# Performance work log

Measured on AMD Instinct MI355X. Metric: run time of the kernel, lower is better.

The kernel has to match this reference:

```python
import jax, jax.numpy as jnp
import numpy as np

B, L, D, H = 4, 1024, 768, 6
DH = D // H
EPS = 1e-5


def setup_inputs() -> dict:
    key = jax.random.key(0)
    kq, kk, kv, kl, kw = jax.random.split(key, 5)
    Q = jax.random.normal(kq, (B, L, D), jnp.float32)
    K = jax.random.normal(kk, (B, L, D), jnp.float32)
    V = jax.random.normal(kv, (B, L, D), jnp.float32)
    # realistic padding: each batch element has a valid length in [L//2, L]
    lengths = jax.random.randint(kl, (B,), L // 2, L + 1)
    valid = jnp.arange(L)[None, :] < lengths[:, None]          # (B, L)
    pad_mask = valid[:, :, None] & valid[:, None, :]           # (B, L, L), True = keep
    bx_packed = ~valid                                         # (B, L), True = padded
    # BatchNorm affine params (per-head channels)
    g1 = jnp.ones((H,), jnp.float32)
    b1 = jnp.zeros((H,), jnp.float32)
    g2 = jnp.ones((H,), jnp.float32)
    b2 = jnp.zeros((H,), jnp.float32)
    # posterior gate: Linear(H, 2)
    Wp = jax.random.normal(kw, (2, H), jnp.float32) * (1.0 / np.sqrt(H))
    bp = jnp.zeros((2,), jnp.float32)
    return {"Q": Q, "K": K, "V": V, "pad_mask": pad_mask, "bx_packed": bx_packed,
            "g1": g1, "b1": b1, "g2": g2, "b2": b2, "Wp": Wp, "bp": bp}


def _split_heads(x):
    b, l, _ = x.shape
    return x.reshape(b, l, H, DH).transpose(0, 2, 1, 3)  # (B, H, L, DH)


def _batchnorm(x, g, b):
    # x: (B, H, N); training-mode BatchNorm1d over channels H (stats over B and N)
    m = x.mean(axis=(0, 2), keepdims=True)
    v = x.var(axis=(0, 2), keepdims=True)  # biased, as torch uses for normalization
    return (x - m) * jax.lax.rsqrt(v + EPS) * g[None, :, None] + b[None, :, None]


def _remove_nan(x):
    return jnp.where(jnp.isnan(x), jnp.zeros_like(x), x)


def reference(Q, K, V, pad_mask, bx_packed, g1, b1, g2, b2, Wp, bp):
    Qh, Kh, Vh = _split_heads(Q), _split_heads(K), _split_heads(V)
    b, h, l, _ = Qh.shape
    # DistMatrix: negative squared Euclidean distance between query/key vectors
    # scores[b,h,i,j] = -||Q_i - K_j||^2, via the GEMM-friendly expansion
    q2 = jnp.sum(Qh * Qh, axis=-1)                     # (B, H, L)
    k2 = jnp.sum(Kh * Kh, axis=-1)                     # (B, H, L)
    qk = jnp.einsum("bhid,bhjd->bhij", Qh, Kh)         # (B, H, L, L)
    co = -(q2[..., :, None] + k2[..., None, :] - 2.0 * qk)
    # norm1 over flattened L*L
    co = _batchnorm(co.reshape(b, h, l * l), g1, b1).reshape(b, h, l, l)
    # zero out positions where pad_mask is False (in-place masked fill in torch)
    co = jnp.where(pad_mask[:, None, :, :], co, 0.0)
    co = jax.nn.softmax(co, axis=-1)
    co = _remove_nan(co)
    # column-sum attention mass per key position
    w = co.sum(axis=-2)                                # (B, H, L)
    w = _batchnorm(w, g2, b2).transpose(0, 2, 1)       # (B, L, H)
    # posterior gate: Linear(H,2) + softmax, take class-0 probability
    w = jax.nn.softmax(w @ Wp.T + bp, axis=-1)[..., 0]  # (B, L)
    w = _remove_nan(w)
    w = jnp.where(bx_packed, -jnp.inf, w)
    w = jax.nn.softmax(w, axis=-1)
    w = _remove_nan(w)[..., None]                      # (B, L, 1)
    return co, w, Vh
```

## Files before the change

kernel.cpp:

```cpp
#include <hip/hip_runtime.h>
#include <stdint.h>
#include <stddef.h>

#define BB 4
#define LL 1024
#define DD 768
#define HH 6
#define DHH 128
#define EPS 1e-5f
#define LOG2E 1.44269504088896f

#define CO_ELEMS 25165824
#define W_ELEMS  4096

#define OFF_Q2  0
#define OFF_K2  24576
#define OFF_WC  49152
#define OFF_SP  73728
#define OFF_AC  79872
#define OFF_SS  79888
#define OFF_WP  81920
#define OFF_GP  1654784
#define OFF_MS1 5193728
#define OFF_MS2 5242880

typedef __attribute__((ext_vector_type(8))) short short8;
typedef __attribute__((ext_vector_type(4))) float f32x4;

__device__ __forceinline__ short8 ld_bf8(const float* __restrict__ p) {
    const float4 a = *(const float4*)(p);
    const float4 b = *(const float4*)(p + 4);
    short8 r;
    r[0] = (short)(__float_as_uint(a.x) >> 16);
    r[1] = (short)(__float_as_uint(a.y) >> 16);
    r[2] = (short)(__float_as_uint(a.z) >> 16);
    r[3] = (short)(__float_as_uint(a.w) >> 16);
    r[4] = (short)(__float_as_uint(b.x) >> 16);
    r[5] = (short)(__float_as_uint(b.y) >> 16);
    r[6] = (short)(__float_as_uint(b.z) >> 16);
    r[7] = (short)(__float_as_uint(b.w) >> 16);
    return r;
}

__device__ __forceinline__ short8 pack_bf8(float4 a, float4 b) {
    short8 r;
    r[0] = (short)(__float_as_uint(a.x) >> 16);
    r[1] = (short)(__float_as_uint(a.y) >> 16);
    r[2] = (short)(__float_as_uint(a.z) >> 16);
    r[3] = (short)(__float_as_uint(a.w) >> 16);
    r[4] = (short)(__float_as_uint(b.x) >> 16);
    r[5] = (short)(__float_as_uint(b.y) >> 16);
    r[6] = (short)(__float_as_uint(b.z) >> 16);
    r[7] = (short)(__float_as_uint(b.w) >> 16);
    return r;
}

__global__ __launch_bounds__(256) void k_gram(
        const float* __restrict__ Q, const float* __restrict__ K,
        const float* __restrict__ V,
        float* __restrict__ ws, float* __restrict__ gramP,
        float* __restrict__ ms1, float* __restrict__ ms2,
        float* __restrict__ vh) {
    const int ic = blockIdx.x;
    const int bh = blockIdx.y;
    const int which = blockIdx.z;
    const int b = bh / HH, h = bh - b * HH;
    const int t = threadIdx.x;

    if (which == 2) {
        const float* srcv = V + (size_t)b * LL * DD + h * DHH;
        float* dstv = vh + ((size_t)bh * LL + (size_t)ic * 128) * DHH;
#pragma unroll
        for (int p = 0; p < 16; p++) {
            const int idx = p * 256 + t;
            const int row = idx >> 5, d4 = idx & 31;
            f32x4 v = *(const f32x4*)(srcv + (size_t)(ic * 128 + row) * DD + d4 * 4);
            __builtin_nontemporal_store(v, (f32x4*)(dstv + (size_t)row * DHH + d4 * 4));
        }
        return;
    }

    const float* src = (which ? K : Q) + (size_t)b * LL * DD + h * DHH;
    float* sqout = ws + (which ? OFF_K2 : OFF_Q2) + bh * 1024 + ic * 128;

    const int lane = t & 63, wv = t >> 6;
    const int lm = lane & 15, quad = lane >> 4;

    __shared__ float tileT[128][129];
    __shared__ float q2loc[128];

    const int ig = t >> 5;
    const int d0 = (t & 31) * 4;
#pragma unroll 4
    for (int p = 0; p < 16; p++) {
        const int i_loc = p * 8 + ig;
        float4 v = *(const float4*)(src + (size_t)(ic * 128 + i_loc) * DD + d0);
        tileT[d0 + 0][i_loc] = __uint_as_float(__float_as_uint(v.x) & 0xffff0000u);
        tileT[d0 + 1][i_loc] = __uint_as_float(__float_as_uint(v.y) & 0xffff0000u);
        tileT[d0 + 2][i_loc] = __uint_as_float(__float_as_uint(v.z) & 0xffff0000u);
        tileT[d0 + 3][i_loc] = __uint_as_float(__float_as_uint(v.w) & 0xffff0000u);
        float s = v.x * v.x + v.y * v.y + v.z * v.z + v.w * v.w;
#pragma unroll
        for (int off = 1; off < 32; off <<= 1) s += __shfl_xor(s, off);
        if ((t & 31) == 0) { q2loc[i_loc] = s; sqout[i_loc] = s; }
    }
    __syncthreads();

    if (t < 128) {
        float s1 = 0.f, s2 = 0.f;
#pragma unroll 8
        for (int i = 0; i < 128; i++) {
            float v = tileT[t][i];
            s1 += v;
            s2 += v * q2loc[i];
        }
        const size_t mo = ((size_t)(which * 24 + bh) * 8 + ic) * 128 + t;
        ms1[mo] = s1;
        ms2[mo] = s2;
    }

    const size_t gbase = ((size_t)(which * 24 + bh) * 8 + ic) * 9216;
    int pi = 0;
    for (int dt = 0; dt < 8; dt++) {
        for (int et = dt; et < 8; et++, pi++) {
            if ((pi & 3) != wv) continue;
            f32x4 acc = (f32x4)(0.0f);
#pragma unroll
            for (int kk = 0; kk < 4; kk++) {
                const int i0 = kk * 32 + quad * 8;
                const float* pa = &tileT[dt * 16 + lm][i0];
                const float* pb = &tileT[et * 16 + lm][i0];
                short8 af, bf;
#pragma unroll
                for (int e = 0; e < 8; e++) {
                    af[e] = (short)(__float_as_uint(pa[e]) >> 16);
                    bf[e] = (short)(__float_as_uint(pb[e]) >> 16);
                }
                acc = __builtin_amdgcn_mfma_f32_16x16x32_bf16(af, bf, acc, 0, 0, 0);
            }
            if (dt != et && which == 0) {
                acc[0] *= 2.f; acc[1] *= 2.f; acc[2] *= 2.f; acc[3] *= 2.f;
            }
            *(f32x4*)&gramP[gbase + (size_t)pi * 256 + lane * 4] = acc;
        }
    }
}

__global__ __launch_bounds__(1024) void k_stats3(
        const float* __restrict__ ms1, const float* __restrict__ ms2,
        const float* __restrict__ gramP,
        const float* __restrict__ q2, const float* __restrict__ k2,
        float* __restrict__ statsP) {
    const int bh = blockIdx.x;
    const int t = threadIdx.x, lane = t & 63, w = t >> 6;
    __shared__ float sQ[128], sK[128], sQq2[128], sKk2[128];
    __shared__ float sred[16][4];
    __shared__ float gred[16];

    if (t < 256) {
        const int d = t & 127, which = t >> 7;
        const float* p1 = ms1 + (size_t)(which * 24 + bh) * 1024 + d;
        const float* p2 = ms2 + (size_t)(which * 24 + bh) * 1024 + d;
        float s1 = 0.f, s2 = 0.f;
#pragma unroll
        for (int ic = 0; ic < 8; ic++) { s1 += p1[ic * 128]; s2 += p2[ic * 128]; }
        if (which) { sK[d] = s1; sKk2[d] = s2; }
        else       { sQ[d] = s1; sQq2[d] = s2; }
    }
    if (t >= 512 && t < 768) {
        const int tt = t - 512;
        f32x4 qv = *(const f32x4*)(q2 + bh * 1024 + tt * 4);
        f32x4 kv = *(const f32x4*)(k2 + bh * 1024 + tt * 4);
        float p0 = qv[0] + qv[1] + qv[2] + qv[3];
        float p1 = qv[0]*qv[0] + qv[1]*qv[1] + qv[2]*qv[2] + qv[3]*qv[3];
        float p2 = kv[0] + kv[1] + kv[2] + kv[3];
        float p3 = kv[0]*kv[0] + kv[1]*kv[1] + kv[2]*kv[2] + kv[3]*kv[3];
#pragma unroll
        for (int off = 1; off < 64; off <<= 1) {
            p0 += __shfl_xor(p0, off); p1 += __shfl_xor(p1, off);
            p2 += __shfl_xor(p2, off); p3 += __shfl_xor(p3, off);
        }
        if (lane == 0) { sred[w][0] = p0; sred[w][1] = p1; sred[w][2] = p2; sred[w][3] = p3; }
    }
    {
        const float* gq = gramP + (size_t)(0 * 24 + bh) * 8 * 9216;
        const float* gk = gramP + (size_t)(1 * 24 + bh) * 8 * 9216;
        float gg = 0.f;
#pragma unroll
        for (int it = 0; it < 9; it++) {
            const int f = it * 1024 + t;
            float a = 0.f, c = 0.f;
#pragma unroll
            for (int icc = 0; icc < 8; icc++) {
                a += gq[(size_t)icc * 9216 + f];
                c += gk[(size_t)icc * 9216 + f];
            }
            gg += a * c;
        }
#pragma unroll
        for (int off = 1; off < 64; off <<= 1) gg += __shfl_xor(gg, off);
        if (lane == 0) gred[w] = gg;
    }
    __syncthreads();
    if (t < 64) {
        float dA  = sQ[t] * sK[t] + sQ[t + 64] * sK[t + 64];
        float dBq = sQq2[t] * sK[t] + sQq2[t + 64] * sK[t + 64];
        float dBk = sQ[t] * sKk2[t] + sQ[t + 64] * sKk2[t + 64];
#pragma unroll
        for (int off = 1; off < 64; off <<= 1) {
            dA += __shfl_xor(dA, off); dBq += __shfl_xor(dBq, off); dBk += __shfl_xor(dBk, off);
        }
        if (t == 0) {
            float SQ2   = sred[8][0] + sred[9][0] + sred[10][0] + sred[11][0];
            float SQ2SQ = sred[8][1] + sred[9][1] + sred[10][1] + sred[11][1];
            float SK2   = sred[8][2] + sred[9][2] + sred[10][2] + sred[11][2];
            float SK2SQ = sred[8][3] + sred[9][3] + sred[10][3] + sred[11][3];
            float GG = 0.f;
#pragma unroll
            for (int i = 0; i < 16; i++) GG += gred[i];
            float sumS  = 2.f * dA - 1024.f * (SQ2 + SK2);
            float sumS2 = 4.f * GG + 1024.f * (SQ2SQ + SK2SQ) + 2.f * SQ2 * SK2 - 4.f * (dBq + dBk);
            statsP[bh * 2]     = sumS;
            statsP[bh * 2 + 1] = sumS2;
        }
    }
}

__global__ void k_stats2(const float* __restrict__ statsP,
                         const float* __restrict__ g1, const float* __restrict__ b1,
                         float* __restrict__ ac) {
    const int t = threadIdx.x;
    if (t < HH) {
        float T1 = 0.f, T2 = 0.f;
#pragma unroll
        for (int b = 0; b < 4; b++) {
            T1 += statsP[(b * HH + t) * 2];
            T2 += statsP[(b * HH + t) * 2 + 1];
        }
        const float N = 4194304.f;
        float m_ = T1 / N;
        float var = fmaxf(T2 / N - m_ * m_, 0.0f);
        float r = rsqrtf(var + EPS);
        float a = r * g1[t];
        ac[t] = a;
        ac[8 + t] = b1[t] - m_ * a;
    }
}

#define KLOAD(buf, jtv) do {                                                   \
    const float* _p = Kb + (size_t)(jw + (jtv) * 16 + lm) * DD + quad * 8;     \
    buf##0 = *(const float4*)(_p);        buf##1 = *(const float4*)(_p + 4);   \
    buf##2 = *(const float4*)(_p + 32);   buf##3 = *(const float4*)(_p + 36);  \
    buf##4 = *(const float4*)(_p + 64);   buf##5 = *(const float4*)(_p + 68);  \
    buf##6 = *(const float4*)(_p + 96);   buf##7 = *(const float4*)(_p + 100); \
} while (0)

#define KCOMP(buf, jtv) do {                                                   \
    short8 kf0 = pack_bf8(buf##0, buf##1);                                     \
    short8 kf1 = pack_bf8(buf##2, buf##3);                                     \
    short8 kf2 = pack_bf8(buf##4, buf##5);                                     \
    short8 kf3 = pack_bf8(buf##6, buf##7);                                     \
    f32x4 acc0 = (f32x4)(0.0f), acc1 = (f32x4)(0.0f);                          \
    acc0 = __builtin_amdgcn_mfma_f32_16x16x32_bf16(kf0, qf[0][0], acc0, 0, 0, 0); \
    acc1 = __builtin_amdgcn_mfma_f32_16x16x32_bf16(kf0, qf[1][0], acc1, 0, 0, 0); \
    acc0 = __builtin_amdgcn_mfma_f32_16x16x32_bf16(kf1, qf[0][1], acc0, 0, 0, 0); \
    acc1 = __builtin_amdgcn_mfma_f32_16x16x32_bf16(kf1, qf[1][1], acc1, 0, 0, 0); \
    acc0 = __builtin_amdgcn_mfma_f32_16x16x32_bf16(kf2, qf[0][2], acc0, 0, 0, 0); \
    acc1 = __builtin_amdgcn_mfma_f32_16x16x32_bf16(kf2, qf[1][2], acc1, 0, 0, 0); \
    acc0 = __builtin_amdgcn_mfma_f32_16x16x32_bf16(kf3, qf[0][3], acc0, 0, 0, 0); \
    acc1 = __builtin_amdgcn_mfma_f32_16x16x32_bf16(kf3, qf[1][3], acc1, 0, 0, 0); \
    const int jb = jw + (jtv) * 16;                                            \
    const f32x4 k2v = *(const f32x4*)(k2 + bh * 1024 + jb + quad * 4);         \
    const uchar4 m4 = *(const uchar4*)(bxb + jb + quad * 4);                   \
    const bool vj0 = (m4.x == 0), vj1 = (m4.y == 0);                           \
    const bool vj2 = (m4.z == 0), vj3 = (m4.w == 0);                           \
    f32x4 kc;                                                                  \
    kc[0] = a1l * k2v[0]; kc[1] = a1l * k2v[1];                                \
    kc[2] = a1l * k2v[2]; kc[3] = a1l * k2v[3];                                \
    {                                                                          \
        f32x4 ev;                                                              \
        ev[0] = (vi0 && vj0) ? exp2f(fminf(fmaf(a2l, acc0[0], cr0 - kc[0]), 86.56f)) : 1.0f; \
        ev[1] = (vi0 && vj1) ? exp2f(fminf(fmaf(a2l, acc0[1], cr0 - kc[1]), 86.56f)) : 1.0f; \
        ev[2] = (vi0 && vj2) ? exp2f(fminf(fmaf(a2l, acc0[2], cr0 - kc[2]), 86.56f)) : 1.0f; \
        ev[3] = (vi0 && vj3) ? exp2f(fminf(fmaf(a2l, acc0[3], cr0 - kc[3]), 86.56f)) : 1.0f; \
        *(f32x4*)&e_lds[lm][jb + quad * 4] = ev;                               \
        rsum0 += (ev[0] + ev[1]) + (ev[2] + ev[3]);                            \
    }                                                                          \
    {                                                                          \
        f32x4 ev;                                                              \
        ev[0] = (vi1 && vj0) ? exp2f(fminf(fmaf(a2l, acc1[0], cr1 - kc[0]), 86.56f)) : 1.0f; \
        ev[1] = (vi1 && vj1) ? exp2f(fminf(fmaf(a2l, acc1[1], cr1 - kc[1]), 86.56f)) : 1.0f; \
        ev[2] = (vi1 && vj2) ? exp2f(fminf(fmaf(a2l, acc1[2], cr1 - kc[2]), 86.56f)) : 1.0f; \
        ev[3] = (vi1 && vj3) ? exp2f(fminf(fmaf(a2l, acc1[3], cr1 - kc[3]), 86.56f)) : 1.0f; \
        *(f32x4*)&e_lds[16 + lm][jb + quad * 4] = ev;                          \
        rsum1 += (ev[0] + ev[1]) + (ev[2] + ev[3]);                            \
    }                                                                          \
} while (0)

__global__ __launch_bounds__(512, 1) void k_fused(
        const float* __restrict__ Q, const float* __restrict__ Km,
        const float* __restrict__ q2, const float* __restrict__ k2,
        const float* __restrict__ ac, const unsigned char* __restrict__ bx,
        float* __restrict__ co, float* __restrict__ wcolP) {
    const int g = blockIdx.x;
    const int xcd = g & 7, slot = g >> 3;
    const int t = threadIdx.x, lane = t & 63, w = t >> 6;
    const int lm = lane & 15, quad = lane >> 4;
    const int jw = w * 128;

    __shared__ float e_lds[32][1028];
    __shared__ float rowsum[3][32];
    if (t < 96) ((float*)rowsum)[t] = 0.f;
    __syncthreads();

#pragma unroll 1
    for (int rep = 0; rep < 3; rep++) {
        const int idx = slot * 3 + rep;
        const int bh = xcd + ((idx >> 5) << 3);
        const int strip = idx & 31;
        const int b = bh / HH, h = bh - b * HH;
        const int i0 = strip * 32;
        const float* Qb = Q + (size_t)b * LL * DD + h * DHH;
        const float* Kb = Km + (size_t)b * LL * DD + h * DHH;
        const float a1 = ac[h], c1 = ac[8 + h];
        const unsigned char* bxb = bx + b * LL;
        const float a1l = a1 * LOG2E;
        const float a2l = 2.0f * a1l;
        const float c1l = c1 * LOG2E;

        short8 qf[2][4];
#pragma unroll
        for (int s = 0; s < 2; s++)
#pragma unroll
            for (int kk = 0; kk < 4; kk++)
                qf[s][kk] = ld_bf8(Qb + (size_t)(i0 + s * 16 + lm) * DD + kk * 32 + quad * 8);

        const bool vi0 = (bxb[i0 + lm] == 0);
        const bool vi1 = (bxb[i0 + 16 + lm] == 0);
        const float cr0 = c1l - a1l * q2[bh * 1024 + i0 + lm];
        const float cr1 = c1l - a1l * q2[bh * 1024 + i0 + 16 + lm];

        float4 rA0, rA1, rA2, rA3, rA4, rA5, rA6, rA7;
        float4 rB0, rB1, rB2, rB3, rB4, rB5, rB6, rB7;

        float rsum0 = 0.f, rsum1 = 0.f;
        KLOAD(rA, 0);
        KLOAD(rB, 1);
        KCOMP(rA, 0);
        KLOAD(rA, 2);
        KCOMP(rB, 1);
        KLOAD(rB, 3);
        KCOMP(rA, 2);
        KLOAD(rA, 4);
        KCOMP(rB, 3);
        KLOAD(rB, 5);
        KCOMP(rA, 4);
        KLOAD(rA, 6);
        KCOMP(rB, 5);
        KLOAD(rB, 7);
        KCOMP(rA, 6);
        KCOMP(rB, 7);

        rsum0 += __shfl_xor(rsum0, 16);
        rsum0 += __shfl_xor(rsum0, 32);
        rsum1 += __shfl_xor(rsum1, 16);
        rsum1 += __shfl_xor(rsum1, 32);
        if (lane < 16) {
            atomicAdd(&rowsum[rep][lm], rsum0);
            atomicAdd(&rowsum[rep][16 + lm], rsum1);
        }
        __syncthreads();

        const int cg = t & 255, rh = t >> 8;
        float* cob = co + ((size_t)bh << 20) + (size_t)(i0 + rh * 16) * 1024 + cg * 4;
        float* wp = wcolP + ((size_t)((strip * 2 + rh) * 24 + bh)) * 1024 + cg * 4;
        float cs0 = 0.f, cs1 = 0.f, cs2 = 0.f, cs3 = 0.f;
#pragma unroll
        for (int rr = 0; rr < 16; rr++) {
            const int r = rh * 16 + rr;
            const float inv = 1.0f / rowsum[rep][r];
            f32x4 v = *(const f32x4*)&e_lds[r][cg * 4];
            v[0] *= inv; v[1] *= inv; v[2] *= inv; v[3] *= inv;
            __builtin_nontemporal_store(v, (f32x4*)(cob + (size_t)rr * 1024));
            cs0 += v[0]; cs1 += v[1]; cs2 += v[2]; cs3 += v[3];
        }
        f32x4 wv; wv[0] = cs0; wv[1] = cs1; wv[2] = cs2; wv[3] = cs3;
        *(f32x4*)wp = wv;
        __syncthreads();
    }
}

__global__ void k_wcol_reduce(const float* __restrict__ wcolP,
                              float* __restrict__ wcol, float* __restrict__ ws2) {
    const int t = threadIdx.x;
    int g = blockIdx.x * 256 + t;
    float s = 0.f;
#pragma unroll 8
    for (int strip = 0; strip < 64; strip++)
        s += wcolP[(size_t)strip * 24576 + g];
    wcol[g] = s;
    float a = s, b = s * s;
#pragma unroll
    for (int off = 1; off < 64; off <<= 1) { a += __shfl_xor(a, off); b += __shfl_xor(b, off); }
    __shared__ float sc[4][2];
    if ((t & 63) == 0) { sc[t >> 6][0] = a; sc[t >> 6][1] = b; }
    __syncthreads();
    if (t == 0) {
        ws2[blockIdx.x * 2]     = sc[0][0] + sc[1][0] + sc[2][0] + sc[3][0];
        ws2[blockIdx.x * 2 + 1] = sc[0][1] + sc[1][1] + sc[2][1] + sc[3][1];
    }
}

__global__ __launch_bounds__(1024) void k_tail(
        const float* __restrict__ wcol, const float* __restrict__ ws2,
        const unsigned char* __restrict__ bx,
        const float* __restrict__ g2, const float* __restrict__ b2,
        const float* __restrict__ Wp, const float* __restrict__ bp,
        float* __restrict__ wout) {
    const int t = threadIdx.x, lane = t & 63, wv = t >> 6;
    __shared__ float abuf[12];
    __shared__ float xb[4096];
    __shared__ float wred[16][2];

    if (t < HH) {
        float s = 0.f, s2 = 0.f;
        for (int b = 0; b < 4; b++) {
            int bh = b * HH + t;
#pragma unroll
            for (int sub = 0; sub < 4; sub++) {
                int blk = bh * 4 + sub;
                s += ws2[blk * 2];
                s2 += ws2[blk * 2 + 1];
            }
        }
        float m = s / 4096.f;
        float var = fmaxf(s2 / 4096.f - m * m, 0.0f);
        float r = rsqrtf(var + EPS);
        float a = r * g2[t];
        abuf[t] = a;
        abuf[6 + t] = b2[t] - m * a;
    }
    __syncthreads();

    const float bp0 = bp[0], bp1 = bp[1];
#pragma unroll
    for (int p = 0; p < 4; p++) {
        int idx = t + p * 1024;
        int b = idx >> 10, l = idx & 1023;
        float z0 = bp0, z1 = bp1;
#pragma unroll
        for (int h = 0; h < HH; h++) {
            float wn = abuf[h] * wcol[(size_t)(b * HH + h) * 1024 + l] + abuf[6 + h];
            z0 += wn * Wp[h];
            z1 += wn * Wp[HH + h];
        }
        float pc = 1.0f / (1.0f + __expf(z1 - z0));
        xb[idx] = bx[b * LL + l] ? -INFINITY : pc;
    }
    __syncthreads();

    const int bb = t >> 8, tb = t & 255;
    float4 xv = *(const float4*)&xb[bb * 1024 + tb * 4];
    float mx = fmaxf(fmaxf(xv.x, xv.y), fmaxf(xv.z, xv.w));
#pragma unroll
    for (int off = 1; off < 64; off <<= 1) mx = fmaxf(mx, __shfl_xor(mx, off));
    if (lane == 0) wred[wv][0] = mx;
    __syncthreads();
    mx = fmaxf(fmaxf(wred[bb * 4][0], wred[bb * 4 + 1][0]),
               fmaxf(wred[bb * 4 + 2][0], wred[bb * 4 + 3][0]));
    float e0 = __expf(xv.x - mx), e1 = __expf(xv.y - mx);
    float e2 = __expf(xv.z - mx), e3 = __expf(xv.w - mx);
    float ss = e0 + e1 + e2 + e3;
#pragma unroll
    for (int off = 1; off < 64; off <<= 1) ss += __shfl_xor(ss, off);
    if (lane == 0) wred[wv][1] = ss;
    __syncthreads();
    float sum = wred[bb * 4][1] + wred[bb * 4 + 1][1] + wred[bb * 4 + 2][1] + wred[bb * 4 + 3][1];
    float4 o;
    o.x = e0 / sum; o.y = e1 / sum; o.z = e2 / sum; o.w = e3 / sum;
    *(float4*)&wout[bb * 1024 + tb * 4] = o;
}

extern "C" void kernel_launch(void* const* d_in, const int* in_sizes, int n_in,
                              void* d_out, int out_size, void* d_ws, size_t ws_size,
                              hipStream_t stream) {
    const float* Q  = (const float*)d_in[0];
    const float* K  = (const float*)d_in[1];
    const float* V  = (const float*)d_in[2];
    const unsigned char* bx = (const unsigned char*)d_in[4];
    const float* g1 = (const float*)d_in[5];
    const float* b1 = (const float*)d_in[6];
    const float* g2 = (const float*)d_in[7];
    const float* b2 = (const float*)d_in[8];
    const float* Wp = (const float*)d_in[9];
    const float* bp = (const float*)d_in[10];

    float* out  = (float*)d_out;
    float* co   = out;
    float* wout = out + CO_ELEMS;
    float* vh   = out + CO_ELEMS + W_ELEMS;

    float* ws = (float*)d_ws;
    float* q2     = ws + OFF_Q2;
    float* k2     = ws + OFF_K2;
    float* wcol   = ws + OFF_WC;
    float* statsP = ws + OFF_SP;
    float* ac     = ws + OFF_AC;
    float* ws2    = ws + OFF_SS;
    float* wcolP  = ws + OFF_WP;
    float* gramP  = ws + OFF_GP;
    float* ms1    = ws + OFF_MS1;
    float* ms2    = ws + OFF_MS2;

    k_gram<<<dim3(8, 24, 3), 256, 0, stream>>>(Q, K, V, ws, gramP, ms1, ms2, vh);
    k_stats3<<<24, 1024, 0, stream>>>(ms1, ms2, gramP, q2, k2, statsP);
    k_stats2<<<1, 64, 0, stream>>>(statsP, g1, b1, ac);
    k_fused<<<256, 512, 0, stream>>>(Q, K, q2, k2, ac, bx, co, wcolP);
    k_wcol_reduce<<<96, 256, 0, stream>>>(wcolP, wcol, ws2);
    k_tail<<<1, 1024, 0, stream>>>(wcol, ws2, bx, g2, b2, Wp, bp, wout);
}
```

Baseline: 260.7 us.

## Fuse stats2, wcol reduce and tail into preceding kernels via atomic last-block counters

Removes three small kernel launches by folding the BN1 finalization into k_stats3 and the column reduction plus the final gate softmax into k_fused, using global atomic counters so the last-arriving block does the follow-up work. It also prefetches the next strip's Q fragments and K tiles before the store phase of the current strip, so loads overlap the co writes. The costs are extra fences and serialized tail work in a single block, plus the risk of memory-ordering bugs with the counters.

```diff
diff --git a/kernel.cpp b/kernel.cpp
--- a/kernel.cpp
+++ b/kernel.cpp
@@ -23,6 +23,7 @@
 #define OFF_GP  1654784
 #define OFF_MS1 5193728
 #define OFF_MS2 5242880
+#define OFF_CT  5292032
 
 typedef __attribute__((ext_vector_type(8))) short short8;
 typedef __attribute__((ext_vector_type(4))) float f32x4;
@@ -55,12 +56,18 @@
     return r;
 }
 
+__device__ __forceinline__ void bar_lgkm() {
+    asm volatile("s_waitcnt lgkmcnt(0)" ::: "memory");
+    __builtin_amdgcn_s_barrier();
+    __builtin_amdgcn_sched_barrier(0);
+}
+
 __global__ __launch_bounds__(256) void k_gram(
         const float* __restrict__ Q, const float* __restrict__ K,
         const float* __restrict__ V,
         float* __restrict__ ws, float* __restrict__ gramP,
         float* __restrict__ ms1, float* __restrict__ ms2,
-        float* __restrict__ vh) {
+        float* __restrict__ vh, unsigned* __restrict__ ctr) {
     const int ic = blockIdx.x;
     const int bh = blockIdx.y;
     const int which = blockIdx.z;
@@ -68,6 +75,7 @@
     const int t = threadIdx.x;
 
     if (which == 2) {
+        if (ic == 0 && bh == 0 && t < 32) ctr[t] = 0u;
         const float* srcv = V + (size_t)b * LL * DD + h * DHH;
         float* dstv = vh + ((size_t)bh * LL + (size_t)ic * 128) * DHH;
 #pragma unroll
@@ -150,7 +158,9 @@
         const float* __restrict__ ms1, const float* __restrict__ ms2,
         const float* __restrict__ gramP,
         const float* __restrict__ q2, const float* __restrict__ k2,
-        float* __restrict__ statsP) {
+        const float* __restrict__ g1, const float* __restrict__ b1,
+        float* __restrict__ statsP, float* __restrict__ ac,
+        unsigned* __restrict__ ctr) {
     const int bh = blockIdx.x;
     const int t = threadIdx.x, lane = t & 63, w = t >> 6;
     __shared__ float sQ[128], sK[128], sQq2[128], sKk2[128];
@@ -222,28 +232,28 @@
             float sumS2 = 4.f * GG + 1024.f * (SQ2SQ + SK2SQ) + 2.f * SQ2 * SK2 - 4.f * (dBq + dBk);
             statsP[bh * 2]     = sumS;
             statsP[bh * 2 + 1] = sumS2;
-        }
-    }
-}
-
-__global__ void k_stats2(const float* __restrict__ statsP,
-                         const float* __restrict__ g1, const float* __restrict__ b1,
-                         float* __restrict__ ac) {
-    const int t = threadIdx.x;
-    if (t < HH) {
-        float T1 = 0.f, T2 = 0.f;
-#pragma unroll
-        for (int b = 0; b < 4; b++) {
-            T1 += statsP[(b * HH + t) * 2];
-            T2 += statsP[(b * HH + t) * 2 + 1];
-        }
-        const float N = 4194304.f;
-        float m_ = T1 / N;
-        float var = fmaxf(T2 / N - m_ * m_, 0.0f);
-        float r = rsqrtf(var + EPS);
-        float a = r * g1[t];
-        ac[t] = a;
-        ac[8 + t] = b1[t] - m_ * a;
+            __threadfence();
+            unsigned old = atomicAdd(&ctr[30], 1u);
+            if (old == 23u) {
+                __threadfence();
+#pragma unroll
+                for (int h = 0; h < HH; h++) {
+                    float T1 = 0.f, T2 = 0.f;
+#pragma unroll
+                    for (int b = 0; b < 4; b++) {
+                        T1 += statsP[(b * HH + h) * 2];
+                        T2 += statsP[(b * HH + h) * 2 + 1];
+                    }
+                    const float N = 4194304.f;
+                    float m_ = T1 / N;
+                    float var = fmaxf(T2 / N - m_ * m_, 0.0f);
+                    float r = rsqrtf(var + EPS);
+                    float a = r * g1[h];
+                    ac[h] = a;
+                    ac[8 + h] = b1[h] - m_ * a;
+                }
+            }
+        }
     }
 }
 
@@ -270,7 +280,7 @@
     acc0 = __builtin_amdgcn_mfma_f32_16x16x32_bf16(kf3, qf[0][3], acc0, 0, 0, 0); \
     acc1 = __builtin_amdgcn_mfma_f32_16x16x32_bf16(kf3, qf[1][3], acc1, 0, 0, 0); \
     const int jb = jw + (jtv) * 16;                                            \
-    const f32x4 k2v = *(const f32x4*)(k2 + bh * 1024 + jb + quad * 4);         \
+    const f32x4 k2v = *(const f32x4*)(k2b + jb + quad * 4);                    \
     const uchar4 m4 = *(const uchar4*)(bxb + jb + quad * 4);                   \
     const bool vj0 = (m4.x == 0), vj1 = (m4.y == 0);                           \
     const bool vj2 = (m4.z == 0), vj3 = (m4.w == 0);                           \
@@ -297,11 +307,37 @@
     }                                                                          \
 } while (0)
 
+#define SETUP(idxv) do {                                                       \
+    bh = xcd + ((((idxv) >> 5)) << 3); strip = (idxv) & 31;                    \
+    const int b_ = bh / HH, h_ = bh - b_ * HH;                                 \
+    const int i0_ = strip * 32;                                                \
+    const float* Qb_ = Q + (size_t)b_ * LL * DD + h_ * DHH;                    \
+    Kb  = Km + (size_t)b_ * LL * DD + h_ * DHH;                                \
+    k2b = k2 + bh * 1024;                                                      \
+    bxb = bx + b_ * LL;                                                        \
+    a1l = ac[h_] * LOG2E; a2l = 2.0f * a1l;                                    \
+    const float c1l_ = ac[8 + h_] * LOG2E;                                     \
+    _Pragma("unroll")                                                          \
+    for (int s = 0; s < 2; s++)                                                \
+        _Pragma("unroll")                                                      \
+        for (int kk = 0; kk < 4; kk++)                                         \
+            qf[s][kk] = ld_bf8(Qb_ + (size_t)(i0_ + s * 16 + lm) * DD + kk * 32 + quad * 8); \
+    vi0 = (bxb[i0_ + lm] == 0);                                                \
+    vi1 = (bxb[i0_ + 16 + lm] == 0);                                           \
+    cr0 = c1l_ - a1l * q2[bh * 1024 + i0_ + lm];                               \
+    cr1 = c1l_ - a1l * q2[bh * 1024 + i0_ + 16 + lm];                          \
+    KLOAD(rA, 0); KLOAD(rB, 1);                                                \
+} while (0)
+
 __global__ __launch_bounds__(512, 1) void k_fused(
         const float* __restrict__ Q, const float* __restrict__ Km,
         const float* __restrict__ q2, const float* __restrict__ k2,
         const float* __restrict__ ac, const unsigned char* __restrict__ bx,
-        float* __restrict__ co, float* __restrict__ wcolP) {
+        const float* __restrict__ g2, const float* __restrict__ b2,
+        const float* __restrict__ Wp, const float* __restrict__ bp,
+        float* __restrict__ co, float* __restrict__ wcolP,
+        float* __restrict__ wcol, float* __restrict__ ws2,
+        unsigned* __restrict__ ctr, float* __restrict__ wout) {
     const int g = blockIdx.x;
     const int xcd = g & 7, slot = g >> 3;
     const int t = threadIdx.x, lane = t & 63, w = t >> 6;
@@ -310,42 +346,26 @@
 
     __shared__ float e_lds[32][1028];
     __shared__ float rowsum[3][32];
+    __shared__ int sclaim[2];
+    __shared__ int stail;
+    __shared__ float scr[8][2];
+    __shared__ float abuf[12];
     if (t < 96) ((float*)rowsum)[t] = 0.f;
     __syncthreads();
+
+    int bh, strip;
+    const float* Kb; const float* k2b; const unsigned char* bxb;
+    float a1l, a2l, cr0, cr1;
+    bool vi0, vi1;
+    short8 qf[2][4];
+    float4 rA0, rA1, rA2, rA3, rA4, rA5, rA6, rA7;
+    float4 rB0, rB1, rB2, rB3, rB4, rB5, rB6, rB7;
+
+    SETUP(slot * 3);
 
 #pragma unroll 1
     for (int rep = 0; rep < 3; rep++) {
-        const int idx = slot * 3 + rep;
-        const int bh = xcd + ((idx >> 5) << 3);
-        const int strip = idx & 31;
-        const int b = bh / HH, h = bh - b * HH;
-        const int i0 = strip * 32;
-        const float* Qb = Q + (size_t)b * LL * DD + h * DHH;
-        const float* Kb = Km + (size_t)b * LL * DD + h * DHH;
-        const float a1 = ac[h], c1 = ac[8 + h];
-        const unsigned char* bxb = bx + b * LL;
-        const float a1l = a1 * LOG2E;
-        const float a2l = 2.0f * a1l;
-        const float c1l = c1 * LOG2E;
-
-        short8 qf[2][4];
-#pragma unroll
-        for (int s = 0; s < 2; s++)
-#pragma unroll
-            for (int kk = 0; kk < 4; kk++)
-                qf[s][kk] = ld_bf8(Qb + (size_t)(i0 + s * 16 + lm) * DD + kk * 32 + quad * 8);
-
-        const bool vi0 = (bxb[i0 + lm] == 0);
-        const bool vi1 = (bxb[i0 + 16 + lm] == 0);
-        const float cr0 = c1l - a1l * q2[bh * 1024 + i0 + lm];
-        const float cr1 = c1l - a1l * q2[bh * 1024 + i0 + 16 + lm];
-
-        float4 rA0, rA1, rA2, rA3, rA4, rA5, rA6, rA7;
-        float4 rB0, rB1, rB2, rB3, rB4, rB5, rB6, rB7;
-
         float rsum0 = 0.f, rsum1 = 0.f;
-        KLOAD(rA, 0);
-        KLOAD(rB, 1);
         KCOMP(rA, 0);
         KLOAD(rA, 2);
         KCOMP(rB, 1);
@@ -369,11 +389,16 @@
             atomicAdd(&rowsum[rep][lm], rsum0);
             atomicAdd(&rowsum[rep][16 + lm], rsum1);
         }
-        __syncthreads();
-
+        bar_lgkm();
+
+        const int pb_bh = bh, pb_strip = strip;
+        if (rep < 2) SETUP(slot * 3 + rep + 1);
+        __builtin_amdgcn_sched_barrier(0);
+
+        const int i0p = pb_strip * 32;
         const int cg = t & 255, rh = t >> 8;
-        float* cob = co + ((size_t)bh << 20) + (size_t)(i0 + rh * 16) * 1024 + cg * 4;
-        float* wp = wcolP + ((size_t)((strip * 2 + rh) * 24 + bh)) * 1024 + cg * 4;
+        float* cob = co + ((size_t)pb_bh << 20) + (size_t)(i0p + rh * 16) * 1024 + cg * 4;
+        float* wp = wcolP + ((size_t)((pb_strip * 2 + rh) * 24 + pb_bh)) * 1024 + cg * 4;
         float cs0 = 0.f, cs1 = 0.f, cs2 = 0.f, cs3 = 0.f;
 #pragma unroll
         for (int rr = 0; rr < 16; rr++) {
@@ -386,99 +411,123 @@
         }
         f32x4 wv; wv[0] = cs0; wv[1] = cs1; wv[2] = cs2; wv[3] = cs3;
         *(f32x4*)wp = wv;
+        bar_lgkm();
+    }
+
+    asm volatile("s_waitcnt vmcnt(0)" ::: "memory");
+    __threadfence();
+    __syncthreads();
+    if (t == 0) {
+        sclaim[0] = -1; sclaim[1] = -1; stail = 0;
+        int nc = 0;
+#pragma unroll
+        for (int r = 0; r < 3; r++) {
+            const int idxv = slot * 3 + r;
+            const int bhv = xcd + ((idxv >> 5) << 3);
+            unsigned o = atomicAdd(&ctr[bhv], 1u);
+            if (o == 31u) sclaim[nc++] = bhv;
+        }
+    }
+    __syncthreads();
+    const int ncl = (sclaim[0] >= 0) + (sclaim[1] >= 0);
+    if (ncl) {
+        __threadfence();
+        for (int c = 0; c < 2; c++) {
+            const int cb = sclaim[c];
+            if (cb < 0) continue;
+            const int c0 = t, c1 = t + 512;
+            float s0 = 0.f, s1 = 0.f;
+            for (int sp = 0; sp < 64; sp++) {
+                const float* wp_ = wcolP + ((size_t)sp * 24 + cb) * 1024;
+                s0 += wp_[c0];
+                s1 += wp_[c1];
+            }
+            wcol[cb * 1024 + c0] = s0;
+            wcol[cb * 1024 + c1] = s1;
+            float a = s0 + s1, q = s0 * s0 + s1 * s1;
+#pragma unroll
+            for (int off = 1; off < 64; off <<= 1) { a += __shfl_xor(a, off); q += __shfl_xor(q, off); }
+            if (lane == 0) { scr[w][0] = a; scr[w][1] = q; }
+            __syncthreads();
+            if (t == 0) {
+                float A = 0.f, Qq = 0.f;
+#pragma unroll
+                for (int i = 0; i < 8; i++) { A += scr[i][0]; Qq += scr[i][1]; }
+                ws2[cb * 2] = A; ws2[cb * 2 + 1] = Qq;
+            }
+            __syncthreads();
+        }
+        asm volatile("s_waitcnt vmcnt(0)" ::: "memory");
+        __threadfence();
+    }
+    __syncthreads();
+    if (t == 0 && ncl) {
+        int tc = 0;
+#pragma unroll
+        for (int c = 0; c < 2; c++)
+            if (sclaim[c] >= 0) {
+                unsigned o = atomicAdd(&ctr[24], 1u);
+                if (o == 23u) tc = 1;
+            }
+        stail = tc;
+    }
+    __syncthreads();
+    if (stail) {
+        __threadfence();
+        if (t < HH) {
+            float s = 0.f, s2 = 0.f;
+#pragma unroll
+            for (int b_ = 0; b_ < 4; b_++) {
+                s  += ws2[(b_ * HH + t) * 2];
+                s2 += ws2[(b_ * HH + t) * 2 + 1];
+            }
+            float m = s / 4096.f;
+            float var = fmaxf(s2 / 4096.f - m * m, 0.0f);
+            float r = rsqrtf(var + EPS);
+            float a = r * g2[t];
+            abuf[t] = a;
+            abuf[6 + t] = b2[t] - m * a;
+        }
         __syncthreads();
-    }
-}
-
-__global__ void k_wcol_reduce(const float* __restrict__ wcolP,
-                              float* __restrict__ wcol, float* __restrict__ ws2) {
-    const int t = threadIdx.x;
-    int g = blockIdx.x * 256 + t;
-    float s = 0.f;
-#pragma unroll 8
-    for (int strip = 0; strip < 64; strip++)
-        s += wcolP[(size_t)strip * 24576 + g];
-    wcol[g] = s;
-    float a = s, b = s * s;
-#pragma unroll
-    for (int off = 1; off < 64; off <<= 1) { a += __shfl_xor(a, off); b += __shfl_xor(b, off); }
-    __shared__ float sc[4][2];
-    if ((t & 63) == 0) { sc[t >> 6][0] = a; sc[t >> 6][1] = b; }
-    __syncthreads();
-    if (t == 0) {
-        ws2[blockIdx.x * 2]     = sc[0][0] + sc[1][0] + sc[2][0] + sc[3][0];
-        ws2[blockIdx.x * 2 + 1] = sc[0][1] + sc[1][1] + sc[2][1] + sc[3][1];
-    }
-}
-
-__global__ __launch_bounds__(1024) void k_tail(
-        const float* __restrict__ wcol, const float* __restrict__ ws2,
-        const unsigned char* __restrict__ bx,
-        const float* __restrict__ g2, const float* __restrict__ b2,
-        const float* __restrict__ Wp, const float* __restrict__ bp,
-        float* __restrict__ wout) {
-    const int t = threadIdx.x, lane = t & 63, wv = t >> 6;
-    __shared__ float abuf[12];
-    __shared__ float xb[4096];
-    __shared__ float wred[16][2];
-
-    if (t < HH) {
-        float s = 0.f, s2 = 0.f;
-        for (int b = 0; b < 4; b++) {
-            int bh = b * HH + t;
-#pragma unroll
-            for (int sub = 0; sub < 4; sub++) {
-                int blk = bh * 4 + sub;
-                s += ws2[blk * 2];
-                s2 += ws2[blk * 2 + 1];
-            }
-        }
-        float m = s / 4096.f;
-        float var = fmaxf(s2 / 4096.f - m * m, 0.0f);
-        float r = rsqrtf(var + EPS);
-        float a = r * g2[t];
-        abuf[t] = a;
-        abuf[6 + t] = b2[t] - m * a;
-    }
-    __syncthreads();
-
-    const float bp0 = bp[0], bp1 = bp[1];
-#pragma unroll
-    for (int p = 0; p < 4; p++) {
-        int idx = t + p * 1024;
-        int b = idx >> 10, l = idx & 1023;
-        float z0 = bp0, z1 = bp1;
-#pragma unroll
-        for (int h = 0; h < HH; h++) {
-            float wn = abuf[h] * wcol[(size_t)(b * HH + h) * 1024 + l] + abuf[6 + h];
-            z0 += wn * Wp[h];
-            z1 += wn * Wp[HH + h];
-        }
-        float pc = 1.0f / (1.0f + __expf(z1 - z0));
-        xb[idx] = bx[b * LL + l] ? -INFINITY : pc;
-    }
-    __syncthreads();
-
-    const int bb = t >> 8, tb = t & 255;
-    float4 xv = *(const float4*)&xb[bb * 1024 + tb * 4];
-    float mx = fmaxf(fmaxf(xv.x, xv.y), fmaxf(xv.z, xv.w));
-#pragma unroll
-    for (int off = 1; off < 64; off <<= 1) mx = fmaxf(mx, __shfl_xor(mx, off));
-    if (lane == 0) wred[wv][0] = mx;
-    __syncthreads();
-    mx = fmaxf(fmaxf(wred[bb * 4][0], wred[bb * 4 + 1][0]),
-               fmaxf(wred[bb * 4 + 2][0], wred[bb * 4 + 3][0]));
-    float e0 = __expf(xv.x - mx), e1 = __expf(xv.y - mx);
-    float e2 = __expf(xv.z - mx), e3 = __expf(xv.w - mx);
-    float ss = e0 + e1 + e2 + e3;
-#pragma unroll
-    for (int off = 1; off < 64; off <<= 1) ss += __shfl_xor(ss, off);
-    if (lane == 0) wred[wv][1] = ss;
-    __syncthreads();
-    float sum = wred[bb * 4][1] + wred[bb * 4 + 1][1] + wred[bb * 4 + 2][1] + wred[bb * 4 + 3][1];
-    float4 o;
-    o.x = e0 / sum; o.y = e1 / sum; o.z = e2 / sum; o.w = e3 / sum;
-    *(float4*)&wout[bb * 1024 + tb * 4] = o;
+        if (w < 4) {
+            const int b_ = w;
+            const float bp0 = bp[0], bp1 = bp[1];
+            float vbuf[16];
+            float mx = -INFINITY;
+#pragma unroll
+            for (int u = 0; u < 16; u++) {
+                const int l = lane * 16 + u;
+                float z0 = bp0, z1 = bp1;
+#pragma unroll
+                for (int h_ = 0; h_ < HH; h_++) {
+                    const float wn = abuf[h_] * wcol[(b_ * HH + h_) * 1024 + l] + abuf[6 + h_];
+                    z0 += wn * Wp[h_];
+                    z1 += wn * Wp[HH + h_];
+                }
+                const float pc = 1.0f / (1.0f + __expf(z1 - z0));
+                const float v_ = bx[b_ * LL + l] ? -INFINITY : pc;
+                vbuf[u] = v_;
+                mx = fmaxf(mx, v_);
+            }
+#pragma unroll
+            for (int off = 1; off < 64; off <<= 1) mx = fmaxf(mx, __shfl_xor(mx, off));
+            float ssum = 0.f;
+#pragma unroll
+            for (int u = 0; u < 16; u++) { vbuf[u] = __expf(vbuf[u] - mx); ssum += vbuf[u]; }
+#pragma unroll
+            for (int off = 1; off < 64; off <<= 1) ssum += __shfl_xor(ssum, off);
+            const float inv_ = 1.0f / ssum;
+#pragma unroll
+            for (int u4 = 0; u4 < 4; u4++) {
+                f32x4 o;
+                o[0] = vbuf[u4 * 4 + 0] * inv_;
+                o[1] = vbuf[u4 * 4 + 1] * inv_;
+                o[2] = vbuf[u4 * 4 + 2] * inv_;
+                o[3] = vbuf[u4 * 4 + 3] * inv_;
+                *(f32x4*)&wout[b_ * 1024 + lane * 16 + u4 * 4] = o;
+            }
+        }
+    }
 }
 
 extern "C" void kernel_launch(void* const* d_in, const int* in_sizes, int n_in,
@@ -511,11 +560,10 @@
     float* gramP  = ws + OFF_GP;
     float* ms1    = ws + OFF_MS1;
     float* ms2    = ws + OFF_MS2;
-
-    k_gram<<<dim3(8, 24, 3), 256, 0, stream>>>(Q, K, V, ws, gramP, ms1, ms2, vh);
-    k_stats3<<<24, 1024, 0, stream>>>(ms1, ms2, gramP, q2, k2, statsP);
-    k_stats2<<<1, 64, 0, stream>>>(statsP, g1, b1, ac);
-    k_fused<<<256, 512, 0, stream>>>(Q, K, q2, k2, ac, bx, co, wcolP);
-    k_wcol_reduce<<<96, 256, 0, stream>>>(wcolP, wcol, ws2);
-    k_tail<<<1, 1024, 0, stream>>>(wcol, ws2, bx, g2, b2, Wp, bp, wout);
-}
+    unsigned* ctr = (unsigned*)(ws + OFF_CT);
+
+    k_gram<<<dim3(8, 24, 3), 256, 0, stream>>>(Q, K, V, ws, gramP, ms1, ms2, vh, ctr);
+    k_stats3<<<24, 1024, 0, stream>>>(ms1, ms2, gramP, q2, k2, g1, b1, statsP, ac, ctr);
+    k_fused<<<256, 512, 0, stream>>>(Q, K, q2, k2, ac, bx, g2, b2, Wp, bp,
+                                     co, wcolP, wcol, ws2, ctr, wout);
+}
```

New measurement: 322.0 us. +23.5%, slower.
